# Performance work log

Hardware: AMD Instinct MI355X
Metric: run time of the kernel (lower is better)

## Reference

```python
import jax, jax.numpy as jnp
import numpy as np
from jax import lax

B, N, NUM_CLASSES = 16, 48384, 1
CONF_THRESH = 0.25
IOU_THRESH = 0.45
MAX_PER_IMG = 100
K = 512           # NMS candidate pool (top-K by score)
IMG_SIZE = 1536.0
CLS_OFFSET = 4096.0  # class-aware NMS offset trick


def setup_inputs() -> dict:
    key = jax.random.key(0)
    k1, k2, k3 = jax.random.split(key, 3)
    # cx, cy in [0, IMG), w, h in [0, 0.2*IMG)
    coords = jax.random.uniform(k1, (B, N, 4)) * jnp.array(
        [IMG_SIZE, IMG_SIZE, 0.2 * IMG_SIZE, 0.2 * IMG_SIZE], dtype=jnp.float32)
    confs = jax.random.uniform(k2, (B, N, 1 + NUM_CLASSES))  # obj + class scores in [0,1)
    pred_boxes = jnp.concatenate([coords, confs], axis=-1)   # [B, N, 6]
    features = jax.random.normal(k3, (B, 256, 48, 48), dtype=jnp.float32)
    return {"pred_boxes": pred_boxes, "features": features}


def _iou_matrix(boxes):
    # boxes: [K, 4] xyxy -> [K, K] pairwise IoU
    area = jnp.clip(boxes[:, 2] - boxes[:, 0], 0.0) * jnp.clip(boxes[:, 3] - boxes[:, 1], 0.0)
    lt = jnp.maximum(boxes[:, None, :2], boxes[None, :, :2])
    rb = jnp.minimum(boxes[:, None, 2:], boxes[None, :, 2:])
    wh = jnp.clip(rb - lt, 0.0)
    inter = wh[..., 0] * wh[..., 1]
    return inter / (area[:, None] + area[None, :] - inter + 1e-9)


def _find_thresh(scores, t0):
    # Retry loop of the wrapper: lower conf_thresh until >=1 box passes the conf mask.
    s = lax.stop_gradient(scores)
    def cond(t):
        return jnp.sum(s >= t) == 0
    def body(t):
        return jnp.maximum(t - 0.1, t / 10.0)
    return lax.while_loop(cond, body, t0)


def _postprocess_one(pred, thresh):
    # pred: [N, 5+num_classes]
    cx, cy, w, h = pred[:, 0], pred[:, 1], pred[:, 2], pred[:, 3]
    boxes = jnp.stack([cx - w / 2, cy - h / 2, cx + w / 2, cy + h / 2], axis=-1)  # xyxy
    obj = pred[:, 4]
    cls = pred[:, 5:]
    class_conf = jnp.max(cls, axis=-1)
    class_pred = jnp.argmax(cls, axis=-1)
    score = obj * class_conf
    valid = score >= thresh
    cand_score, idx = lax.top_k(jnp.where(valid, score, 0.0), K)
    cboxes = boxes[idx]
    ccls = class_pred[idx]
    cobj = obj[idx]
    cconf = class_conf[idx]
    cvalid = valid[idx]
    # class-aware NMS: offset boxes per class so cross-class pairs never overlap
    off = ccls.astype(boxes.dtype) * CLS_OFFSET
    iou = _iou_matrix(cboxes + off[:, None])  # [K, K]
    ar = jnp.arange(K)
    def body(i, keep):
        sup = keep[i] & (iou[i] > IOU_THRESH) & (ar > i)
        return keep & ~sup
    keep = lax.fori_loop(0, K, body, cvalid)  # greedy NMS (candidates sorted desc)
    final = jnp.where(keep, cand_score, 0.0)
    out_score, oidx = lax.top_k(final, MAX_PER_IMG)
    det = jnp.concatenate(
        [cboxes[oidx], cobj[oidx][:, None], cconf[oidx][:, None],
         ccls[oidx][:, None].astype(boxes.dtype)], axis=-1)  # [max_det, 7]
    kmask = keep[oidx]
    det = jnp.where(kmask[:, None], det, 0.0)
    return det, kmask


def reference(pred_boxes, features):
    obj = pred_boxes[..., 4]
    cconf = jnp.max(pred_boxes[..., 5:], axis=-1)
    scores = obj * cconf  # [B, N]
    t0 = jnp.full((pred_boxes.shape[0],), CONF_THRESH, pred_boxes.dtype)
    thresh = jax.vmap(_find_thresh)(scores, t0)
    det, mask = jax.vmap(_postprocess_one)(pred_boxes, thresh)
    return det, mask, features
```

## Files before the change

kernel.cpp:

```cpp
#include <hip/hip_runtime.h>
#include <stdint.h>

typedef unsigned int u32;
typedef unsigned long long u64;

#define BATCH 16
#define NBOX  48384
#define KC    512
#define MAXDET 100
#define CONF_T 0.25f
#define HCUT   0.75f
#define IOU_T  0.45f
#define DET_FLOATS (BATCH*MAXDET*7)
#define MASK_OFF   DET_FLOATS
#define FEAT_OFF   (DET_FLOATS + BATCH*MAXDET)
#define FEAT_N     (BATCH*256*48*48)
#define FEAT4_N    (FEAT_N/4)

#define CAPH  4096
#define HBUF  160
#define NBINS 64
#define NBLK1 64
#define BOXPB 756

#define F64   (FEAT4_N/64)
#define CSL1  (13*F64)
#define CSL2  (50*F64)
#define CSL3  (56*F64)
#define K1CPB  256
#define K2ACPB 480
#define K2BCPB 384
#define K2CCPB 240

__device__ __forceinline__ u64 xorred_u64(u64 v, int m){
    u32 lo = __shfl_xor((u32)(v & 0xFFFFFFFFull), m, 64);
    u32 hi = __shfl_xor((u32)(v >> 32), m, 64);
    return ((u64)hi << 32) | lo;
}
__device__ __forceinline__ u64 shflxor_u64(u64 v, int j){
    u32 lo = __shfl_xor((u32)(v & 0xFFFFFFFFull), j, 64);
    u32 hi = __shfl_xor((u32)(v >> 32), j, 64);
    return ((u64)hi << 32) | lo;
}
__device__ __forceinline__ u64 shflidx_u64(u64 v, int src){
    u32 lo = (u32)__shfl((int)(u32)(v & 0xFFFFFFFFull), src, 64);
    u32 hi = (u32)__shfl((int)(u32)(v >> 32), src, 64);
    return ((u64)hi << 32) | lo;
}
__device__ __forceinline__ int score_bin(float sc){
    int bin = (int)((sc - 0.75f) * 256.0f);
    return bin > 63 ? 63 : bin;
}

__global__ __launch_bounds__(512) void k1_score(const float* __restrict__ pred,
        u64* __restrict__ hkey, u32* __restrict__ blkcnt, u32* __restrict__ ghist,
        float* __restrict__ blkmax, const float4* __restrict__ feat4,
        float* __restrict__ out, int copyB)
{
    __shared__ u64 s_hb[HBUF];
    __shared__ u32 s_hist[NBINS];
    __shared__ u32 s_hc;
    __shared__ float s_wm[8];

    const int tid = threadIdx.x;

    if ((int)blockIdx.x < copyB){
        const int nthr = copyB * 512;
        float4* dst = reinterpret_cast<float4*>(out + FEAT_OFF);
        for (int i = (int)blockIdx.x*512 + tid; i < CSL1; i += nthr)
            dst[i] = feat4[i];
        return;
    }

    const int sid = (int)blockIdx.x - copyB;
    const int b = sid >> 6, blk = sid & 63;
    if (tid == 0) s_hc = 0u;
    if (tid < NBINS) s_hist[tid] = 0u;
    __syncthreads();

    const float* pb = pred + ((size_t)b*NBOX + (size_t)blk*BOXPB)*6;
    float m = 0.f;
    for (int i = tid; i < BOXPB; i += 512){
        const float2 oc = *(const float2*)(pb + (size_t)i*6 + 4);
        const float sc = oc.x * oc.y;
        m = fmaxf(m, sc);
        if (sc >= HCUT){
            const u32 slot = atomicAdd(&s_hc, 1u);
            const u32 idx = (u32)(blk*BOXPB + i);
            if (slot < (u32)HBUF)
                s_hb[slot] = ((u64)__float_as_uint(sc) << 32) | (u64)(0xFFFFFFFFu - idx);
            atomicAdd(&s_hist[score_bin(sc)], 1u);
        }
    }
    #pragma unroll
    for (int off = 32; off >= 1; off >>= 1) m = fmaxf(m, __shfl_xor(m, off, 64));
    if ((tid & 63) == 0) s_wm[tid >> 6] = m;
    __syncthreads();
    if (tid == 0){
        float mm = s_wm[0];
        #pragma unroll
        for (int w = 1; w < 8; w++) mm = fmaxf(mm, s_wm[w]);
        blkmax[sid] = mm;
        blkcnt[sid] = s_hc;
    }
    if (tid < NBINS) ghist[(size_t)sid*NBINS + tid] = s_hist[tid];
    const u32 hn = (s_hc < (u32)HBUF ? s_hc : (u32)HBUF);
    for (u32 i = tid; i < hn; i += 512)
        hkey[(size_t)sid*HBUF + i] = s_hb[i];
}

__global__ void copy_kernel(const float4* __restrict__ src, float4* __restrict__ dst){
    int stride = gridDim.x * blockDim.x;
    for (int i = blockIdx.x*blockDim.x + threadIdx.x; i < FEAT4_N; i += stride)
        dst[i] = src[i];
}

__global__ __launch_bounds__(512) void k2a_sel(
        const float* __restrict__ pred, const u64* __restrict__ hkey,
        const u32* __restrict__ blkcnt, u32* ghist ,
        const float* __restrict__ blkmax,
        const float4* __restrict__ feat4, float* __restrict__ out, int copyB)
{
    __shared__ u64 s_list[CAPH];
    __shared__ u64 s_key[KC];
    __shared__ u32 s_scr[1024];
    __shared__ u64 s_tie[256];
    __shared__ u32 s_eqidx[256];
    __shared__ u32 s_pfx[64], s_cnt[64];
    __shared__ float s_thresh;
    __shared__ u32 s_Mh, s_maxc, s_pivbin, s_need, s_fastok;
    __shared__ u32 s_prefix, s_k, s_cntgt, s_cnteq;
    __shared__ int s_vM;

    const int tid = threadIdx.x;

    if ((int)blockIdx.x >= BATCH){
        const int nthr = copyB * 512;
        float4* dst = reinterpret_cast<float4*>(out + FEAT_OFF);
        for (int i = CSL1 + ((int)blockIdx.x - BATCH)*512 + tid; i < CSL2; i += nthr)
            dst[i] = feat4[i];
        return;
    }

    const int b = blockIdx.x;
    const float* predb = pred + (size_t)b*NBOX*6;

    {
        if (tid < 64){
            float vv = blkmax[b*NBLK1 + tid];
            #pragma unroll
            for (int off = 32; off >= 1; off >>= 1) vv = fmaxf(vv, __shfl_xor(vv, off, 64));
            if (tid == 0){
                float t = CONF_T; int g = 0;
                while (vv < t && g < 256){ t = fmaxf(t - 0.1f, t * 0.1f); g++; }
                s_thresh = t;
                s_cntgt = 0u; s_cnteq = 0u; s_fastok = 0u;
            }
        } else if (tid < 128){
            const int l = tid - 64;
            u32 c = blkcnt[b*NBLK1 + l];
            s_cnt[l] = c;
            u32 p = c;
            #pragma unroll
            for (int off = 1; off < 64; off <<= 1){
                u32 o = __shfl_up(p, off, 64);
                if (l >= off) p += o;
            }
            s_pfx[l] = p - c;
            u32 mc = c;
            #pragma unroll
            for (int off = 32; off >= 1; off >>= 1) mc = (u32)max(mc, __shfl_xor(mc, off, 64));
            if (l == 63) s_Mh = p;
            if (l == 0)  s_maxc = mc;
        }
    }
    __syncthreads();
    const u32 Mh = s_Mh;
    const bool fastm = (Mh >= (u32)KC) && (Mh <= (u32)CAPH) && (s_maxc <= (u32)HBUF);

    if (fastm){
        const int wv = tid >> 6, ln = tid & 63;
        #pragma unroll
        for (int q = 0; q < 8; q++){
            const int s = wv + q*8;
            const u32 n = s_cnt[s], base = s_pfx[s];
            const u64* src = hkey + (size_t)(b*NBLK1 + s)*HBUF;
            for (u32 i = ln; i < n; i += 64) s_list[base + i] = src[i];
        }
        const int j = tid & 63, g = tid >> 6;
        const u32* gh = ghist + (size_t)b*NBLK1*NBINS;
        u32 acc = 0;
        #pragma unroll
        for (int r = 0; r < 8; r++) acc += gh[(g + r*8)*64 + j];
        s_scr[g*64 + j] = acc;
    }
    __syncthreads();
    if (fastm && tid < 64){
        u32 h = 0;
        #pragma unroll
        for (int g = 0; g < 8; g++) h += s_scr[g*64 + tid];
        u32 c = h;
        #pragma unroll
        for (int off = 1; off < 64; off <<= 1){
            u32 o = __shfl_down(c, off, 64);
            c += (tid + off < 64) ? o : 0u;
        }
        const u32 above = c - h;
        if (above < (u32)KC && above + h >= (u32)KC){
            s_pivbin = (u32)tid;
            s_need = (u32)KC - above;
            s_fastok = (h <= 256u) ? 1u : 0u;
        }
    }
    __syncthreads();
    const bool fsel = fastm && (s_fastok != 0u);

    if (fsel){
        const u32 pb = s_pivbin;
        const u32 lane = (u32)(tid & 63);
        const u64 below = (1ull << lane) - 1ull;
        for (u32 i0 = 0; i0 < Mh; i0 += 512){
            const u32 i = i0 + (u32)tid;
            const bool inr = (i < Mh);
            const u64 key = inr ? s_list[i] : 0ull;
            u32 j2 = 0u;
            if (inr){
                const float sc = __uint_as_float((u32)(key >> 32));
                j2 = (u32)score_bin(sc);
            }
            const bool isgt = inr && (j2 > pb);
            const bool iseq = inr && (j2 == pb);
            const u64 mg = __ballot(isgt);
            const u64 me = __ballot(iseq);
            u32 bg = 0u, be = 0u;
            if (lane == 0u){
                bg = atomicAdd(&s_cntgt, (u32)__popcll(mg));
                be = atomicAdd(&s_cnteq, (u32)__popcll(me));
            }
            bg = (u32)__shfl((int)bg, 0, 64);
            be = (u32)__shfl((int)be, 0, 64);
            if (isgt){
                const u32 sl = bg + (u32)__popcll(mg & below);
                if (sl < (u32)KC) s_key[sl] = key;
            } else if (iseq){
                const u32 e = be + (u32)__popcll(me & below);
                if (e < 256u) s_tie[e] = key;
            }
        }
        __syncthreads();
        {
            const u32 g0v = (s_cntgt < (u32)KC) ? s_cntgt : (u32)KC;
            u32 ecv = (s_cnteq < 256u) ? s_cnteq : 256u;
            u32 needv = (s_need < ecv) ? s_need : ecv;
            if (tid < (int)ecv){
                const u64 me2 = s_tie[tid];
                u32 r = 0;
                for (u32 u2 = 0; u2 < ecv; ++u2) r += (s_tie[u2] > me2) ? 1u : 0u;
                if (r < needv && g0v + r < (u32)KC) s_key[g0v + r] = me2;
            }
            for (int i = (int)(g0v + needv) + tid; i < KC; i += 512) s_key[i] = 0ull;
        }
        __syncthreads();
    } else {
        const float thresh = s_thresh;
        const u32 base8 = __float_as_uint(thresh) >> 24;
        u32 (*s_hist4)[256] = reinterpret_cast<u32(*)[256]>(s_scr);
        {
            u64 c0=0, c1=0, c2=0, c3=0;
            for (int i = tid; i < NBOX; i += 512){
                const float* pp = predb + (size_t)i*6;
                float sc = pp[4] * pp[5];
                if (sc >= thresh){
                    u32 d = (__float_as_uint(sc) >> 24) - base8; if (d > 15u) d = 15u;
                    u64 inc = 1ull << (16*(d & 3u)); u32 q = d >> 2;
                    c0 += (q==0u)?inc:0ull; c1 += (q==1u)?inc:0ull;
                    c2 += (q==2u)?inc:0ull; c3 += (q==3u)?inc:0ull;
                }
            }
            #pragma unroll
            for (int off = 32; off >= 1; off >>= 1){
                c0 += xorred_u64(c0,off); c1 += xorred_u64(c1,off);
                c2 += xorred_u64(c2,off); c3 += xorred_u64(c3,off);
            }
            u64* warr = s_key;
            if ((tid & 63) == 0){
                int w = tid >> 6;
                warr[w*4+0]=c0; warr[w*4+1]=c1; warr[w*4+2]=c2; warr[w*4+3]=c3;
            }
            __syncthreads();
            if (tid < 16){
                u32 tot = 0;
                #pragma unroll
                for (int w = 0; w < 8; w++){
                    u64 vv = warr[w*4 + (tid >> 2)];
                    tot += (u32)((vv >> (16*(tid & 3))) & 0xFFFFull);
                }
                s_hist4[0][tid] = tot;
            }
            __syncthreads();
            if (tid == 0){
                u32 h[16]; u32 tot = 0;
                #pragma unroll
                for (int d = 0; d < 16; d++){ h[d] = s_hist4[0][d]; tot += h[d]; }
                s_vM = (int)tot;
                s_k = KC; s_prefix = 0u;
                if (tot > (u32)KC){
                    u32 k = KC, c = 0; int d = 15;
                    for (; d >= 0; --d){ if (c + h[d] >= k) break; c += h[d]; }
                    if (d < 0) d = 0;
                    s_prefix = (base8 + (u32)d) << 24; s_k = k - c;
                }
            }
            __syncthreads();
        }
        const int vM = s_vM;
        if (vM > KC){
            for (int shift = 16; shift >= 0; shift -= 8){
                for (int z = tid; z < 1024; z += 512) ((u32*)s_hist4)[z] = 0u;
                __syncthreads();
                const u32 prefix = s_prefix;
                const u32 pmask = 0xFFFFFFFFu << (shift + 8);
                const int cpy = tid >> 8;
                for (int i = tid; i < NBOX; i += 512){
                    const float* pp = predb + (size_t)i*6;
                    float sc = pp[4] * pp[5];
                    if (sc >= thresh){
                        u32 bb = __float_as_uint(sc);
                        if ((bb & pmask) == (prefix & pmask))
                            atomicAdd(&s_hist4[cpy][(bb >> shift) & 0xFFu], 1u);
                    }
                }
                __syncthreads();
                if (tid < 256)
                    s_hist4[0][tid] = s_hist4[0][tid] + s_hist4[1][tid]
                                    + s_hist4[2][tid] + s_hist4[3][tid];
                __syncthreads();
                if (tid < 64){
                    const int l = tid;
                    u32 h0 = s_hist4[0][4*l+0], h1 = s_hist4[0][4*l+1];
                    u32 h2 = s_hist4[0][4*l+2], h3 = s_hist4[0][4*l+3];
                    u32 mysum = h0+h1+h2+h3;
                    u32 c = mysum;
                    #pragma unroll
                    for (int off = 1; off < 64; off <<= 1){
                        u32 o = __shfl_down(c, off, 64);
                        c += (l + off < 64) ? o : 0u;
                    }
                    u32 a3 = c - mysum;
                    u32 a2 = a3 + h3, a1 = a2 + h2, a0 = a1 + h1;
                    u32 k = s_k;
                    int sel = -1; u32 cab = 0;
                    if (a0 < k && a0 + h0 >= k){ sel = 0; cab = a0; }
                    if (a1 < k && a1 + h1 >= k){ sel = 1; cab = a1; }
                    if (a2 < k && a2 + h2 >= k){ sel = 2; cab = a2; }
                    if (a3 < k && a3 + h3 >= k){ sel = 3; cab = a3; }
                    if (sel >= 0){
                        s_prefix = prefix | ((u32)(4*l + sel) << shift);
                        s_k = k - cab;
                    }
                }
                __syncthreads();
            }
        }
        const u32 pivot = (vM > KC) ? s_prefix : 0u;
        const bool pivot0 = (vM <= KC);
        const int kneed = pivot0 ? 0 : (int)s_k;
        for (int i = tid; i < NBOX; i += 512){
            const float* pp = predb + (size_t)i*6;
            float sc = pp[4] * pp[5];
            if (sc < thresh) continue;
            u32 bb = __float_as_uint(sc);
            if (bb > pivot){
                u32 sl = atomicAdd(&s_cntgt, 1u);
                if (sl < (u32)KC) s_key[sl] = ((u64)bb << 32) | (u64)(0xFFFFFFFFu - (u32)i);
            } else if (!pivot0 && bb == pivot){
                u32 e = atomicAdd(&s_cnteq, 1u);
                if (e < 256u) s_eqidx[e] = (u32)i;
            }
        }
        __syncthreads();
        if (tid == 0){
            int g = (int)s_cntgt; if (g > KC) g = KC;
            int ec = (int)s_cnteq; if (ec > 256) ec = 256;
            int need = kneed < ec ? kneed : ec;
            for (int t = 0; t < need; t++){
                int mi = t;
                for (int u = t+1; u < ec; u++) if (s_eqidx[u] < s_eqidx[mi]) mi = u;
                u32 tmp = s_eqidx[mi]; s_eqidx[mi] = s_eqidx[t]; s_eqidx[t] = tmp;
                if (g < KC) s_key[g++] = ((u64)pivot << 32) | (u64)(0xFFFFFFFFu - tmp);
            }
            while (g < KC) s_key[g++] = 0ull;
        }
        __syncthreads();
    }

    u64 v = s_key[tid];
    {
        #define CAS_W(kk, j) \
            { \
                u64 p = shflxor_u64(v, (j)); \
                bool keepMax = (((tid & (kk)) == 0) == ((tid & (j)) == 0)); \
                u64 mx = (v > p) ? v : p, mn = (v > p) ? p : v; \
                v = keepMax ? mx : mn; \
            }
        #define CAS_L(kk, j) \
            __syncthreads(); \
            s_key[tid] = v; \
            __syncthreads(); \
            { \
                u64 p = s_key[tid ^ (j)]; \
                bool keepMax = (((tid & (kk)) == 0) == ((tid & (j)) == 0)); \
                u64 mx = (v > p) ? v : p, mn = (v > p) ? p : v; \
                v = keepMax ? mx : mn; \
            }
        CAS_W(2,1)
        CAS_W(4,2)  CAS_W(4,1)
        CAS_W(8,4)  CAS_W(8,2)  CAS_W(8,1)
        CAS_W(16,8) CAS_W(16,4) CAS_W(16,2) CAS_W(16,1)
        CAS_W(32,16) CAS_W(32,8) CAS_W(32,4) CAS_W(32,2) CAS_W(32,1)
        CAS_W(64,32) CAS_W(64,16) CAS_W(64,8) CAS_W(64,4) CAS_W(64,2) CAS_W(64,1)
        CAS_L(128,64)
        CAS_W(128,32) CAS_W(128,16) CAS_W(128,8) CAS_W(128,4) CAS_W(128,2) CAS_W(128,1)
        CAS_L(256,128) CAS_L(256,64)
        CAS_W(256,32) CAS_W(256,16) CAS_W(256,8) CAS_W(256,4) CAS_W(256,2) CAS_W(256,1)
        CAS_L(512,256) CAS_L(512,128) CAS_L(512,64)
        CAS_W(512,32) CAS_W(512,16) CAS_W(512,8) CAS_W(512,4) CAS_W(512,2) CAS_W(512,1)
        #undef CAS_W
        #undef CAS_L
    }

    {
        u32 bb = (u32)(v >> 32);
        u32 idx = 0xFFFFFFFFu - (u32)(v & 0xFFFFFFFFull);
        int srcrow = (bb != 0u) ? (int)idx : 0;
        const float* p = predb + (size_t)srcrow*6;
        const float2 p01 = *(const float2*)(p);
        const float2 p23 = *(const float2*)(p + 2);
        const float2 p45 = *(const float2*)(p + 4);
        float cx = p01.x, cy = p01.y, w = p23.x, h = p23.y, ob = p45.x, cf = p45.y;
        float x1 = cx - w * 0.5f, y1 = cy - h * 0.5f;
        float x2 = cx + w * 0.5f, y2 = cy + h * 0.5f;
        float4* cw = reinterpret_cast<float4*>(ghist) + ((size_t)b*KC + tid)*2;
        cw[0] = make_float4(x1, y1, x2, y2);
        cw[1] = make_float4(fmaxf(x2 - x1, 0.f) * fmaxf(y2 - y1, 0.f),
                            ob, cf, __uint_as_float(bb));
    }
}

__global__ __launch_bounds__(256) void k2b_iou(const float4* __restrict__ cand,
        u64* __restrict__ masks, u64* __restrict__ vmasks,
        const float4* __restrict__ feat4, float* __restrict__ out, int copyB)
{
    __shared__ float4 s_box[KC];
    __shared__ float s_area[KC];
    const int tid = threadIdx.x;

    if ((int)blockIdx.x >= BATCH*9){
        const int nthr = copyB * 256;
        float4* dst = reinterpret_cast<float4*>(out + FEAT_OFF);
        for (int i = CSL2 + ((int)blockIdx.x - BATCH*9)*256 + tid; i < CSL3; i += nthr)
            dst[i] = feat4[i];
        return;
    }

    const int b = (int)blockIdx.x / 9, q = (int)blockIdx.x % 9;
    const float4* cb = cand + (size_t)b*KC*2;

    for (int i = tid; i < KC; i += 256){
        s_box[i] = cb[2*i];
        s_area[i] = cb[2*i+1].x;
    }
    __syncthreads();

    const int wv = tid >> 6, lane = tid & 63;
    const int p = q*4 + wv;
    int d = 0; while ((d+1)*(d+2)/2 <= p) d++;
    const int c = p - d*(d+1)/2;
    const int j = d*64 + lane;
    const float4 bj = s_box[j];
    const float aj = s_area[j];
    const bool isdiag = (c == d);
    u64 acc = 0ull;
    for (int t = 0; t < 64; t++){
        const float4 bi = s_box[c*64 + t];
        const float ai = s_area[c*64 + t];
        float lx = fmaxf(bi.x, bj.x), ly = fmaxf(bi.y, bj.y);
        float rx = fminf(bi.z, bj.z), ry = fminf(bi.w, bj.w);
        float iw = fmaxf(rx - lx, 0.f), ih = fmaxf(ry - ly, 0.f);
        float inter = iw * ih;
        float denom = ai + aj - inter + 1e-9f;
        const bool iouc = (inter > IOU_T * denom);
        bool setb = isdiag ? (iouc && t > lane) : iouc;
        acc |= setb ? (1ull << t) : 0ull;
    }
    if (isdiag) vmasks[(size_t)b*KC + c*64 + lane] = acc;
    else        masks[(size_t)b*4096 + (size_t)c*512 + j] = acc;
}

__global__ __launch_bounds__(512) void k2c_nms(const float4* __restrict__ cand,
        const u64* __restrict__ masks, const u64* __restrict__ vmasks,
        float* __restrict__ out,
        const float4* __restrict__ feat4, int copyB)
{
    __shared__ u64 s_masks[8];
    __shared__ u32 s_wpcnt[8], s_wpfx[8];
    __shared__ int s_outidx[MAXDET];
    __shared__ int s_outcnt;

    const int tid = threadIdx.x;

    if ((int)blockIdx.x >= BATCH){
        const int nthr = copyB * 512;
        float4* dst = reinterpret_cast<float4*>(out + FEAT_OFF);
        for (int i = CSL3 + ((int)blockIdx.x - BATCH)*512 + tid; i < FEAT4_N; i += nthr)
            dst[i] = feat4[i];
        return;
    }

    const int b = blockIdx.x;
    const int wave = tid >> 6, lane = tid & 63;
    const float4* cb = cand + (size_t)b*KC*2;
    const u64* mb = masks + (size_t)b*4096;

    const float4 meta = cb[2*tid + 1];
    const bool alive0 = (__float_as_uint(meta.w) != 0u);
    const u64 vm = vmasks[(size_t)b*KC + tid];
    u64 pre[7];
    #pragma unroll
    for (int e = 0; e < 7; e++) pre[e] = (e < wave) ? mb[(size_t)e*512 + tid] : 0ull;

    for (int c = 0; c < 8; c++){
        if (wave == c){
            bool alive = alive0;
            #pragma unroll
            for (int e = 0; e < 7; e++)
                if (e < c) alive = alive && ((pre[e] & s_masks[e]) == 0ull);
            u64 A = __ballot(alive);
            #pragma unroll
            for (int t = 0; t < 64; t++){
                const u64 m = shflidx_u64(vm, t);
                if ((A >> t) & 1ull) A &= ~m;
            }
            if (lane == 0) s_masks[c] = A;
        }
        __syncthreads();
    }

    if (tid < 8) s_wpcnt[tid] = (u32)__popcll(s_masks[tid]);
    __syncthreads();
    if (tid == 0){
        u32 run = 0;
        #pragma unroll
        for (int w = 0; w < 8; w++){ s_wpfx[w] = run; run += s_wpcnt[w]; }
        s_outcnt = (int)(run < MAXDET ? run : MAXDET);
    }
    __syncthreads();
    {
        const u64 wd = s_masks[wave];
        if ((wd >> lane) & 1ull){
            u32 rank = s_wpfx[wave] + (u32)__popcll(wd & ((1ull << lane) - 1ull));
            if (rank < MAXDET) s_outidx[rank] = tid;
        }
    }
    __syncthreads();
    if (tid < MAXDET){
        const int obase = (b * MAXDET + tid) * 7;
        if (tid < s_outcnt){
            int c = s_outidx[tid];
            float4 bx = cb[2*c];
            float4 mt = cb[2*c + 1];
            out[obase+0] = bx.x; out[obase+1] = bx.y;
            out[obase+2] = bx.z; out[obase+3] = bx.w;
            out[obase+4] = mt.y; out[obase+5] = mt.z;
            out[obase+6] = 0.f;
            out[MASK_OFF + b*MAXDET + tid] = 1.f;
        } else {
            #pragma unroll
            for (int q = 0; q < 7; q++) out[obase+q] = 0.f;
            out[MASK_OFF + b*MAXDET + tid] = 0.f;
        }
    }
}

extern "C" void kernel_launch(void* const* d_in, const int* in_sizes, int n_in,
                              void* d_out, int out_size, void* d_ws, size_t ws_size,
                              hipStream_t stream) {
    (void)in_sizes; (void)n_in; (void)out_size;
    const float* pred = (const float*)d_in[0];
    const float* feat = (const float*)d_in[1];
    float* out = (float*)d_out;

    const size_t hkeyBytes = (size_t)BATCH * NBLK1 * HBUF * 8;
    const size_t cntBytes  = (size_t)BATCH * NBLK1 * 4;
    const size_t histBytes = (size_t)BATCH * NBLK1 * NBINS * 4;
    const size_t maxBytes  = (size_t)BATCH * NBLK1 * 4;
    const size_t needBytes = hkeyBytes + cntBytes + histBytes + maxBytes;

    char* base; bool fused;
    if (ws_size >= needBytes){ base = (char*)d_ws; fused = true; }
    else { base = (char*)(out + FEAT_OFF); fused = false; }

    u64* hkeyp  = (u64*)base;
    u32* blkcnt = (u32*)(base + hkeyBytes);
    u32* ghist  = (u32*)(base + hkeyBytes + cntBytes);
    float* blkmax = (float*)(base + hkeyBytes + cntBytes + histBytes);
    float4* cand = (float4*)ghist;
    u64* masks   = hkeyp;
    u64* vmasks  = hkeyp + (size_t)BATCH*4096;

    if (fused){
        k1_score<<<dim3(K1CPB + BATCH*NBLK1), dim3(512), 0, stream>>>(
            pred, hkeyp, blkcnt, ghist, blkmax, (const float4*)feat, out, K1CPB);
        k2a_sel<<<dim3(BATCH + K2ACPB), dim3(512), 0, stream>>>(
            pred, hkeyp, blkcnt, ghist, blkmax, (const float4*)feat, out, K2ACPB);
        k2b_iou<<<dim3(BATCH*9 + K2BCPB), dim3(256), 0, stream>>>(
            cand, masks, vmasks, (const float4*)feat, out, K2BCPB);
        k2c_nms<<<dim3(BATCH + K2CCPB), dim3(512), 0, stream>>>(
            cand, masks, vmasks, out, (const float4*)feat, K2CCPB);
    } else {
        k1_score<<<dim3(BATCH*NBLK1), dim3(512), 0, stream>>>(
            pred, hkeyp, blkcnt, ghist, blkmax, (const float4*)feat, out, 0);
        k2a_sel<<<dim3(BATCH), dim3(512), 0, stream>>>(
            pred, hkeyp, blkcnt, ghist, blkmax, (const float4*)feat, out, 0);
        k2b_iou<<<dim3(BATCH*9), dim3(256), 0, stream>>>(
            cand, masks, vmasks, (const float4*)feat, out, 0);
        k2c_nms<<<dim3(BATCH), dim3(512), 0, stream>>>(
            cand, masks, vmasks, out, (const float4*)feat, 0);
        copy_kernel<<<dim3(1024), dim3(256), 0, stream>>>(
            (const float4*)feat, (float4*)(out + FEAT_OFF));
    }
}
```

Measured before the change: 134.3 us.

## Fuse selection, IoU mask and NMS kernels into one with per-batch flag sync

Merges the top-K selection, pairwise IoU bitmask, and greedy NMS kernels into one kernel. Each image gets 8 blocks that all redo the selection: seven compute off-diagonal IoU mask tiles and signal an atomic flag, while the lead block computes the diagonal masks and spins on that flag before running NMS. The feature copy is also repartitioned across two launches instead of four. This removes two kernel launches and the global candidate round trip. The cost is redundant selection work across 8 blocks per image and a spin-wait that assumes all blocks of an image are resident together.

Result: slower. 150.5 us (+12.1%).

```diff
diff --git a/kernel.cpp b/kernel.cpp
--- a/kernel.cpp
+++ b/kernel.cpp
@@ -22,15 +22,12 @@
 #define NBINS 64
 #define NBLK1 64
 #define BOXPB 756
+#define NCOMP 8
 
 #define F64   (FEAT4_N/64)
-#define CSL1  (13*F64)
-#define CSL2  (50*F64)
-#define CSL3  (56*F64)
-#define K1CPB  256
-#define K2ACPB 480
-#define K2BCPB 384
-#define K2CCPB 240
+#define CSLK1 (24*F64)
+#define K1CPB 256
+#define K2CPB 384
 
 __device__ __forceinline__ u64 xorred_u64(u64 v, int m){
     u32 lo = __shfl_xor((u32)(v & 0xFFFFFFFFull), m, 64);
@@ -54,8 +51,8 @@
 
 __global__ __launch_bounds__(512) void k1_score(const float* __restrict__ pred,
         u64* __restrict__ hkey, u32* __restrict__ blkcnt, u32* __restrict__ ghist,
-        float* __restrict__ blkmax, const float4* __restrict__ feat4,
-        float* __restrict__ out, int copyB)
+        float* __restrict__ blkmax, u32* __restrict__ flags,
+        const float4* __restrict__ feat4, float* __restrict__ out, int copyB)
 {
     __shared__ u64 s_hb[HBUF];
     __shared__ u32 s_hist[NBINS];
@@ -67,13 +64,14 @@
     if ((int)blockIdx.x < copyB){
         const int nthr = copyB * 512;
         float4* dst = reinterpret_cast<float4*>(out + FEAT_OFF);
-        for (int i = (int)blockIdx.x*512 + tid; i < CSL1; i += nthr)
+        for (int i = (int)blockIdx.x*512 + tid; i < CSLK1; i += nthr)
             dst[i] = feat4[i];
         return;
     }
 
     const int sid = (int)blockIdx.x - copyB;
     const int b = sid >> 6, blk = sid & 63;
+    if (sid == 0 && tid < BATCH) flags[tid] = 0u;
     if (tid == 0) s_hc = 0u;
     if (tid < NBINS) s_hist[tid] = 0u;
     __syncthreads();
@@ -115,10 +113,11 @@
         dst[i] = src[i];
 }
 
-__global__ __launch_bounds__(512) void k2a_sel(
+__global__ __launch_bounds__(512) void k2_fused(
         const float* __restrict__ pred, const u64* __restrict__ hkey,
-        const u32* __restrict__ blkcnt, u32* ghist ,
+        const u32* __restrict__ blkcnt, const u32* __restrict__ ghist,
         const float* __restrict__ blkmax,
+        u64* __restrict__ masks, u32* __restrict__ flags,
         const float4* __restrict__ feat4, float* __restrict__ out, int copyB)
 {
     __shared__ u64 s_list[CAPH];
@@ -127,23 +126,32 @@
     __shared__ u64 s_tie[256];
     __shared__ u32 s_eqidx[256];
     __shared__ u32 s_pfx[64], s_cnt[64];
+    __shared__ float4 s_box[KC];
+    __shared__ float s_area[KC];
+    __shared__ float s_obj[KC];
+    __shared__ float s_conf[KC];
+    __shared__ u64 s_masks[8];
+    __shared__ u32 s_wpcnt[8], s_wpfx[8];
+    __shared__ int s_outidx[MAXDET];
     __shared__ float s_thresh;
     __shared__ u32 s_Mh, s_maxc, s_pivbin, s_need, s_fastok;
     __shared__ u32 s_prefix, s_k, s_cntgt, s_cnteq;
-    __shared__ int s_vM;
+    __shared__ int s_vM, s_outcnt;
 
     const int tid = threadIdx.x;
 
-    if ((int)blockIdx.x >= BATCH){
+    if ((int)blockIdx.x >= BATCH*NCOMP){
         const int nthr = copyB * 512;
         float4* dst = reinterpret_cast<float4*>(out + FEAT_OFF);
-        for (int i = CSL1 + ((int)blockIdx.x - BATCH)*512 + tid; i < CSL2; i += nthr)
+        for (int i = CSLK1 + ((int)blockIdx.x - BATCH*NCOMP)*512 + tid; i < FEAT4_N; i += nthr)
             dst[i] = feat4[i];
         return;
     }
 
-    const int b = blockIdx.x;
+    const int b = (int)blockIdx.x >> 3;
+    const int role = (int)blockIdx.x & 7;
     const float* predb = pred + (size_t)b*NBOX*6;
+    u64* masksb = masks + (size_t)b*4096;
 
     {
         if (tid < 64){
@@ -440,94 +448,69 @@
         float cx = p01.x, cy = p01.y, w = p23.x, h = p23.y, ob = p45.x, cf = p45.y;
         float x1 = cx - w * 0.5f, y1 = cy - h * 0.5f;
         float x2 = cx + w * 0.5f, y2 = cy + h * 0.5f;
-        float4* cw = reinterpret_cast<float4*>(ghist) + ((size_t)b*KC + tid)*2;
-        cw[0] = make_float4(x1, y1, x2, y2);
-        cw[1] = make_float4(fmaxf(x2 - x1, 0.f) * fmaxf(y2 - y1, 0.f),
-                            ob, cf, __uint_as_float(bb));
-    }
-}
-
-__global__ __launch_bounds__(256) void k2b_iou(const float4* __restrict__ cand,
-        u64* __restrict__ masks, u64* __restrict__ vmasks,
-        const float4* __restrict__ feat4, float* __restrict__ out, int copyB)
-{
-    __shared__ float4 s_box[KC];
-    __shared__ float s_area[KC];
-    const int tid = threadIdx.x;
-
-    if ((int)blockIdx.x >= BATCH*9){
-        const int nthr = copyB * 256;
-        float4* dst = reinterpret_cast<float4*>(out + FEAT_OFF);
-        for (int i = CSL2 + ((int)blockIdx.x - BATCH*9)*256 + tid; i < CSL3; i += nthr)
-            dst[i] = feat4[i];
+        s_box[tid] = make_float4(x1, y1, x2, y2);
+        s_area[tid] = fmaxf(x2 - x1, 0.f) * fmaxf(y2 - y1, 0.f);
+        s_obj[tid] = ob; s_conf[tid] = cf;
+    }
+    __syncthreads();
+
+    const int wave = tid >> 6, lane = tid & 63;
+
+    if (role != 0){
+        if (wave < 4){
+            const int p = (role - 1)*4 + wave;
+            int d = 1; while ((d+1)*d/2 <= p) d++;
+            const int c = p - d*(d-1)/2;
+            const int j = d*64 + lane;
+            const float4 bj = s_box[j];
+            const float aj = s_area[j];
+            u64 acc = 0ull;
+            for (int t = 0; t < 64; t++){
+                const float4 bi = s_box[c*64 + t];
+                const float ai = s_area[c*64 + t];
+                float lx = fmaxf(bi.x, bj.x), ly = fmaxf(bi.y, bj.y);
+                float rx = fminf(bi.z, bj.z), ry = fminf(bi.w, bj.w);
+                float iw = fmaxf(rx - lx, 0.f), ih = fmaxf(ry - ly, 0.f);
+                float inter = iw * ih;
+                float denom = ai + aj - inter + 1e-9f;
+                bool sup = (inter > IOU_T * denom);
+                acc |= sup ? (1ull << t) : 0ull;
+            }
+            masksb[(size_t)c*512 + j] = acc;
+        }
+        __threadfence();
+        __syncthreads();
+        if (tid == 0) atomicAdd(&flags[b], 1u);
         return;
     }
 
-    const int b = (int)blockIdx.x / 9, q = (int)blockIdx.x % 9;
-    const float4* cb = cand + (size_t)b*KC*2;
-
-    for (int i = tid; i < KC; i += 256){
-        s_box[i] = cb[2*i];
-        s_area[i] = cb[2*i+1].x;
-    }
-    __syncthreads();
-
-    const int wv = tid >> 6, lane = tid & 63;
-    const int p = q*4 + wv;
-    int d = 0; while ((d+1)*(d+2)/2 <= p) d++;
-    const int c = p - d*(d+1)/2;
-    const int j = d*64 + lane;
-    const float4 bj = s_box[j];
-    const float aj = s_area[j];
-    const bool isdiag = (c == d);
-    u64 acc = 0ull;
-    for (int t = 0; t < 64; t++){
-        const float4 bi = s_box[c*64 + t];
-        const float ai = s_area[c*64 + t];
-        float lx = fmaxf(bi.x, bj.x), ly = fmaxf(bi.y, bj.y);
-        float rx = fminf(bi.z, bj.z), ry = fminf(bi.w, bj.w);
-        float iw = fmaxf(rx - lx, 0.f), ih = fmaxf(ry - ly, 0.f);
-        float inter = iw * ih;
-        float denom = ai + aj - inter + 1e-9f;
-        const bool iouc = (inter > IOU_T * denom);
-        bool setb = isdiag ? (iouc && t > lane) : iouc;
-        acc |= setb ? (1ull << t) : 0ull;
-    }
-    if (isdiag) vmasks[(size_t)b*KC + c*64 + lane] = acc;
-    else        masks[(size_t)b*4096 + (size_t)c*512 + j] = acc;
-}
-
-__global__ __launch_bounds__(512) void k2c_nms(const float4* __restrict__ cand,
-        const u64* __restrict__ masks, const u64* __restrict__ vmasks,
-        float* __restrict__ out,
-        const float4* __restrict__ feat4, int copyB)
-{
-    __shared__ u64 s_masks[8];
-    __shared__ u32 s_wpcnt[8], s_wpfx[8];
-    __shared__ int s_outidx[MAXDET];
-    __shared__ int s_outcnt;
-
-    const int tid = threadIdx.x;
-
-    if ((int)blockIdx.x >= BATCH){
-        const int nthr = copyB * 512;
-        float4* dst = reinterpret_cast<float4*>(out + FEAT_OFF);
-        for (int i = CSL3 + ((int)blockIdx.x - BATCH)*512 + tid; i < FEAT4_N; i += nthr)
-            dst[i] = feat4[i];
-        return;
-    }
-
-    const int b = blockIdx.x;
-    const int wave = tid >> 6, lane = tid & 63;
-    const float4* cb = cand + (size_t)b*KC*2;
-    const u64* mb = masks + (size_t)b*4096;
-
-    const float4 meta = cb[2*tid + 1];
-    const bool alive0 = (__float_as_uint(meta.w) != 0u);
-    const u64 vm = vmasks[(size_t)b*KC + tid];
+    u64 vm = 0ull;
+    {
+        const float4 bj = s_box[wave*64 + lane];
+        const float aj = s_area[wave*64 + lane];
+        for (int t = 0; t < 64; t++){
+            const float4 bi = s_box[wave*64 + t];
+            const float ai = s_area[wave*64 + t];
+            float lx = fmaxf(bi.x, bj.x), ly = fmaxf(bi.y, bj.y);
+            float rx = fminf(bi.z, bj.z), ry = fminf(bi.w, bj.w);
+            float iw = fmaxf(rx - lx, 0.f), ih = fmaxf(ry - ly, 0.f);
+            float inter = iw * ih;
+            float denom = aj + ai - inter + 1e-9f;
+            bool sup = (inter > IOU_T * denom) && (t > lane);
+            vm |= sup ? (1ull << t) : 0ull;
+        }
+    }
+    const bool alive0 = (((u32)(v >> 32)) != 0u);
+
+    if (tid == 0){
+        while (atomicAdd(&flags[b], 0u) < 7u){ }
+    }
+    __syncthreads();
+    __threadfence();
+
     u64 pre[7];
     #pragma unroll
-    for (int e = 0; e < 7; e++) pre[e] = (e < wave) ? mb[(size_t)e*512 + tid] : 0ull;
+    for (int e = 0; e < 7; e++) pre[e] = (e < wave) ? masksb[(size_t)e*512 + tid] : 0ull;
 
     for (int c = 0; c < 8; c++){
         if (wave == c){
@@ -567,11 +550,10 @@
         const int obase = (b * MAXDET + tid) * 7;
         if (tid < s_outcnt){
             int c = s_outidx[tid];
-            float4 bx = cb[2*c];
-            float4 mt = cb[2*c + 1];
+            float4 bx = s_box[c];
             out[obase+0] = bx.x; out[obase+1] = bx.y;
             out[obase+2] = bx.z; out[obase+3] = bx.w;
-            out[obase+4] = mt.y; out[obase+5] = mt.z;
+            out[obase+4] = s_obj[c]; out[obase+5] = s_conf[c];
             out[obase+6] = 0.f;
             out[MASK_OFF + b*MAXDET + tid] = 1.f;
         } else {
@@ -594,7 +576,10 @@
     const size_t cntBytes  = (size_t)BATCH * NBLK1 * 4;
     const size_t histBytes = (size_t)BATCH * NBLK1 * NBINS * 4;
     const size_t maxBytes  = (size_t)BATCH * NBLK1 * 4;
-    const size_t needBytes = hkeyBytes + cntBytes + histBytes + maxBytes;
+    const size_t flagBytes = 64;
+    const size_t maskBytes = (size_t)BATCH * 4096 * 8;
+    const size_t needBytes = hkeyBytes + cntBytes + histBytes + maxBytes
+                           + flagBytes + maskBytes;
 
     char* base; bool fused;
     if (ws_size >= needBytes){ base = (char*)d_ws; fused = true; }
@@ -604,28 +589,21 @@
     u32* blkcnt = (u32*)(base + hkeyBytes);
     u32* ghist  = (u32*)(base + hkeyBytes + cntBytes);
     float* blkmax = (float*)(base + hkeyBytes + cntBytes + histBytes);
-    float4* cand = (float4*)ghist;
-    u64* masks   = hkeyp;
-    u64* vmasks  = hkeyp + (size_t)BATCH*4096;
+    u32* flags  = (u32*)(base + hkeyBytes + cntBytes + histBytes + maxBytes);
+    u64* masks  = (u64*)(base + hkeyBytes + cntBytes + histBytes + maxBytes + flagBytes);
 
     if (fused){
         k1_score<<<dim3(K1CPB + BATCH*NBLK1), dim3(512), 0, stream>>>(
-            pred, hkeyp, blkcnt, ghist, blkmax, (const float4*)feat, out, K1CPB);
-        k2a_sel<<<dim3(BATCH + K2ACPB), dim3(512), 0, stream>>>(
-            pred, hkeyp, blkcnt, ghist, blkmax, (const float4*)feat, out, K2ACPB);
-        k2b_iou<<<dim3(BATCH*9 + K2BCPB), dim3(256), 0, stream>>>(
-            cand, masks, vmasks, (const float4*)feat, out, K2BCPB);
-        k2c_nms<<<dim3(BATCH + K2CCPB), dim3(512), 0, stream>>>(
-            cand, masks, vmasks, out, (const float4*)feat, K2CCPB);
+            pred, hkeyp, blkcnt, ghist, blkmax, flags, (const float4*)feat, out, K1CPB);
+        k2_fused<<<dim3(BATCH*NCOMP + K2CPB), dim3(512), 0, stream>>>(
+            pred, hkeyp, blkcnt, ghist, blkmax, masks, flags,
+            (const float4*)feat, out, K2CPB);
     } else {
         k1_score<<<dim3(BATCH*NBLK1), dim3(512), 0, stream>>>(
-            pred, hkeyp, blkcnt, ghist, blkmax, (const float4*)feat, out, 0);
-        k2a_sel<<<dim3(BATCH), dim3(512), 0, stream>>>(
-            pred, hkeyp, blkcnt, ghist, blkmax, (const float4*)feat, out, 0);
-        k2b_iou<<<dim3(BATCH*9), dim3(256), 0, stream>>>(
-            cand, masks, vmasks, (const float4*)feat, out, 0);
-        k2c_nms<<<dim3(BATCH), dim3(512), 0, stream>>>(
-            cand, masks, vmasks, out, (const float4*)feat, 0);
+            pred, hkeyp, blkcnt, ghist, blkmax, flags, (const float4*)feat, out, 0);
+        k2_fused<<<dim3(BATCH*NCOMP), dim3(512), 0, stream>>>(
+            pred, hkeyp, blkcnt, ghist, blkmax, masks, flags,
+            (const float4*)feat, out, 0);
         copy_kernel<<<dim3(1024), dim3(256), 0, stream>>>(
             (const float4*)feat, (float4*)(out + FEAT_OFF));
     }
```

## Fuse IoU-mask and NMS kernels, stream candidates directly, replace bitonic sort with rank sort

Applied to the files above, without the earlier changes.

Merges the IoU bitmask kernel and the greedy NMS kernel into one launch. Each image's block now computes the 36 triangular 64x64 tiles into shared memory, so the masks no longer round-trip through global memory. The selection kernel scans per-block candidate keys straight from global memory instead of staging them into a shared list first. The 512-element bitonic sort is replaced by an O(K) rank-count scatter per thread. The feature-copy slices are redistributed across the remaining three launches. This removes a kernel launch and global traffic, but IoU work now runs on only 16 blocks instead of 144, and the rank sort does 512 shared reads per thread.

New measurement: 167.7 us. +24.9%, slower.

```diff
diff --git a/kernel.cpp b/kernel.cpp
--- a/kernel.cpp
+++ b/kernel.cpp
@@ -24,22 +24,15 @@
 #define BOXPB 756
 
 #define F64   (FEAT4_N/64)
-#define CSL1  (13*F64)
-#define CSL2  (50*F64)
-#define CSL3  (56*F64)
+#define CSL1  (32*F64)
+#define CSL2  (48*F64)
 #define K1CPB  256
-#define K2ACPB 480
-#define K2BCPB 384
-#define K2CCPB 240
+#define K2ACPB 368
+#define K2BCPB 368
 
 __device__ __forceinline__ u64 xorred_u64(u64 v, int m){
     u32 lo = __shfl_xor((u32)(v & 0xFFFFFFFFull), m, 64);
     u32 hi = __shfl_xor((u32)(v >> 32), m, 64);
-    return ((u64)hi << 32) | lo;
-}
-__device__ __forceinline__ u64 shflxor_u64(u64 v, int j){
-    u32 lo = __shfl_xor((u32)(v & 0xFFFFFFFFull), j, 64);
-    u32 hi = __shfl_xor((u32)(v >> 32), j, 64);
     return ((u64)hi << 32) | lo;
 }
 __device__ __forceinline__ u64 shflidx_u64(u64 v, int src){
@@ -121,12 +114,11 @@
         const float* __restrict__ blkmax,
         const float4* __restrict__ feat4, float* __restrict__ out, int copyB)
 {
-    __shared__ u64 s_list[CAPH];
     __shared__ u64 s_key[KC];
     __shared__ u32 s_scr[1024];
     __shared__ u64 s_tie[256];
     __shared__ u32 s_eqidx[256];
-    __shared__ u32 s_pfx[64], s_cnt[64];
+    __shared__ u32 s_cnt[64];
     __shared__ float s_thresh;
     __shared__ u32 s_Mh, s_maxc, s_pivbin, s_need, s_fastok;
     __shared__ u32 s_prefix, s_k, s_cntgt, s_cnteq;
@@ -160,18 +152,13 @@
             const int l = tid - 64;
             u32 c = blkcnt[b*NBLK1 + l];
             s_cnt[l] = c;
-            u32 p = c;
+            u32 sum = c;
             #pragma unroll
-            for (int off = 1; off < 64; off <<= 1){
-                u32 o = __shfl_up(p, off, 64);
-                if (l >= off) p += o;
-            }
-            s_pfx[l] = p - c;
+            for (int off = 32; off >= 1; off >>= 1) sum += __shfl_xor(sum, off, 64);
             u32 mc = c;
             #pragma unroll
             for (int off = 32; off >= 1; off >>= 1) mc = (u32)max(mc, __shfl_xor(mc, off, 64));
-            if (l == 63) s_Mh = p;
-            if (l == 0)  s_maxc = mc;
+            if (l == 0){ s_Mh = sum; s_maxc = mc; }
         }
     }
     __syncthreads();
@@ -179,14 +166,6 @@
     const bool fastm = (Mh >= (u32)KC) && (Mh <= (u32)CAPH) && (s_maxc <= (u32)HBUF);
 
     if (fastm){
-        const int wv = tid >> 6, ln = tid & 63;
-        #pragma unroll
-        for (int q = 0; q < 8; q++){
-            const int s = wv + q*8;
-            const u32 n = s_cnt[s], base = s_pfx[s];
-            const u64* src = hkey + (size_t)(b*NBLK1 + s)*HBUF;
-            for (u32 i = ln; i < n; i += 64) s_list[base + i] = src[i];
-        }
         const int j = tid & 63, g = tid >> 6;
         const u32* gh = ghist + (size_t)b*NBLK1*NBINS;
         u32 acc = 0;
@@ -217,34 +196,41 @@
 
     if (fsel){
         const u32 pb = s_pivbin;
+        const int wv = tid >> 6;
         const u32 lane = (u32)(tid & 63);
         const u64 below = (1ull << lane) - 1ull;
-        for (u32 i0 = 0; i0 < Mh; i0 += 512){
-            const u32 i = i0 + (u32)tid;
-            const bool inr = (i < Mh);
-            const u64 key = inr ? s_list[i] : 0ull;
-            u32 j2 = 0u;
-            if (inr){
-                const float sc = __uint_as_float((u32)(key >> 32));
-                j2 = (u32)score_bin(sc);
-            }
-            const bool isgt = inr && (j2 > pb);
-            const bool iseq = inr && (j2 == pb);
-            const u64 mg = __ballot(isgt);
-            const u64 me = __ballot(iseq);
-            u32 bg = 0u, be = 0u;
-            if (lane == 0u){
-                bg = atomicAdd(&s_cntgt, (u32)__popcll(mg));
-                be = atomicAdd(&s_cnteq, (u32)__popcll(me));
-            }
-            bg = (u32)__shfl((int)bg, 0, 64);
-            be = (u32)__shfl((int)be, 0, 64);
-            if (isgt){
-                const u32 sl = bg + (u32)__popcll(mg & below);
-                if (sl < (u32)KC) s_key[sl] = key;
-            } else if (iseq){
-                const u32 e = be + (u32)__popcll(me & below);
-                if (e < 256u) s_tie[e] = key;
+        #pragma unroll
+        for (int q = 0; q < 8; q++){
+            const int s = wv*8 + q;
+            const u32 n = s_cnt[s];
+            const u64* src = hkey + (size_t)(b*NBLK1 + s)*HBUF;
+            for (u32 i0 = 0; i0 < n; i0 += 64){
+                const u32 i = i0 + lane;
+                const bool inr = (i < n);
+                const u64 key = inr ? src[i] : 0ull;
+                u32 j2 = 0u;
+                if (inr){
+                    const float sc = __uint_as_float((u32)(key >> 32));
+                    j2 = (u32)score_bin(sc);
+                }
+                const bool isgt = inr && (j2 > pb);
+                const bool iseq = inr && (j2 == pb);
+                const u64 mg = __ballot(isgt);
+                const u64 me = __ballot(iseq);
+                u32 bg = 0u, be = 0u;
+                if (lane == 0u){
+                    bg = atomicAdd(&s_cntgt, (u32)__popcll(mg));
+                    be = atomicAdd(&s_cnteq, (u32)__popcll(me));
+                }
+                bg = (u32)__shfl((int)bg, 0, 64);
+                be = (u32)__shfl((int)be, 0, 64);
+                if (isgt){
+                    const u32 sl = bg + (u32)__popcll(mg & below);
+                    if (sl < (u32)KC) s_key[sl] = key;
+                } else if (iseq){
+                    const u32 e = be + (u32)__popcll(me & below);
+                    if (e < 256u) s_tie[e] = key;
+                }
             }
         }
         __syncthreads();
@@ -394,39 +380,19 @@
         __syncthreads();
     }
 
-    u64 v = s_key[tid];
+    u64 v;
     {
-        #define CAS_W(kk, j) \
-            { \
-                u64 p = shflxor_u64(v, (j)); \
-                bool keepMax = (((tid & (kk)) == 0) == ((tid & (j)) == 0)); \
-                u64 mx = (v > p) ? v : p, mn = (v > p) ? p : v; \
-                v = keepMax ? mx : mn; \
-            }
-        #define CAS_L(kk, j) \
-            __syncthreads(); \
-            s_key[tid] = v; \
-            __syncthreads(); \
-            { \
-                u64 p = s_key[tid ^ (j)]; \
-                bool keepMax = (((tid & (kk)) == 0) == ((tid & (j)) == 0)); \
-                u64 mx = (v > p) ? v : p, mn = (v > p) ? p : v; \
-                v = keepMax ? mx : mn; \
-            }
-        CAS_W(2,1)
-        CAS_W(4,2)  CAS_W(4,1)
-        CAS_W(8,4)  CAS_W(8,2)  CAS_W(8,1)
-        CAS_W(16,8) CAS_W(16,4) CAS_W(16,2) CAS_W(16,1)
-        CAS_W(32,16) CAS_W(32,8) CAS_W(32,4) CAS_W(32,2) CAS_W(32,1)
-        CAS_W(64,32) CAS_W(64,16) CAS_W(64,8) CAS_W(64,4) CAS_W(64,2) CAS_W(64,1)
-        CAS_L(128,64)
-        CAS_W(128,32) CAS_W(128,16) CAS_W(128,8) CAS_W(128,4) CAS_W(128,2) CAS_W(128,1)
-        CAS_L(256,128) CAS_L(256,64)
-        CAS_W(256,32) CAS_W(256,16) CAS_W(256,8) CAS_W(256,4) CAS_W(256,2) CAS_W(256,1)
-        CAS_L(512,256) CAS_L(512,128) CAS_L(512,64)
-        CAS_W(512,32) CAS_W(512,16) CAS_W(512,8) CAS_W(512,4) CAS_W(512,2) CAS_W(512,1)
-        #undef CAS_W
-        #undef CAS_L
+        const u64 me2 = s_key[tid];
+        u32 r = 0;
+        #pragma unroll 8
+        for (int u = 0; u < KC; u++){
+            const u64 o = s_key[u];
+            r += (o > me2 || (o == me2 && u < tid)) ? 1u : 0u;
+        }
+        u64* s_out = reinterpret_cast<u64*>(s_scr);
+        s_out[r] = me2;
+        __syncthreads();
+        v = s_out[tid];
     }
 
     {
@@ -447,61 +413,15 @@
     }
 }
 
-__global__ __launch_bounds__(256) void k2b_iou(const float4* __restrict__ cand,
-        u64* __restrict__ masks, u64* __restrict__ vmasks,
-        const float4* __restrict__ feat4, float* __restrict__ out, int copyB)
+__global__ __launch_bounds__(512) void k2bc_nms(const float4* __restrict__ cand,
+        float* __restrict__ out, const float4* __restrict__ feat4, int copyB)
 {
     __shared__ float4 s_box[KC];
     __shared__ float s_area[KC];
-    const int tid = threadIdx.x;
-
-    if ((int)blockIdx.x >= BATCH*9){
-        const int nthr = copyB * 256;
-        float4* dst = reinterpret_cast<float4*>(out + FEAT_OFF);
-        for (int i = CSL2 + ((int)blockIdx.x - BATCH*9)*256 + tid; i < CSL3; i += nthr)
-            dst[i] = feat4[i];
-        return;
-    }
-
-    const int b = (int)blockIdx.x / 9, q = (int)blockIdx.x % 9;
-    const float4* cb = cand + (size_t)b*KC*2;
-
-    for (int i = tid; i < KC; i += 256){
-        s_box[i] = cb[2*i];
-        s_area[i] = cb[2*i+1].x;
-    }
-    __syncthreads();
-
-    const int wv = tid >> 6, lane = tid & 63;
-    const int p = q*4 + wv;
-    int d = 0; while ((d+1)*(d+2)/2 <= p) d++;
-    const int c = p - d*(d+1)/2;
-    const int j = d*64 + lane;
-    const float4 bj = s_box[j];
-    const float aj = s_area[j];
-    const bool isdiag = (c == d);
-    u64 acc = 0ull;
-    for (int t = 0; t < 64; t++){
-        const float4 bi = s_box[c*64 + t];
-        const float ai = s_area[c*64 + t];
-        float lx = fmaxf(bi.x, bj.x), ly = fmaxf(bi.y, bj.y);
-        float rx = fminf(bi.z, bj.z), ry = fminf(bi.w, bj.w);
-        float iw = fmaxf(rx - lx, 0.f), ih = fmaxf(ry - ly, 0.f);
-        float inter = iw * ih;
-        float denom = ai + aj - inter + 1e-9f;
-        const bool iouc = (inter > IOU_T * denom);
-        bool setb = isdiag ? (iouc && t > lane) : iouc;
-        acc |= setb ? (1ull << t) : 0ull;
-    }
-    if (isdiag) vmasks[(size_t)b*KC + c*64 + lane] = acc;
-    else        masks[(size_t)b*4096 + (size_t)c*512 + j] = acc;
-}
-
-__global__ __launch_bounds__(512) void k2c_nms(const float4* __restrict__ cand,
-        const u64* __restrict__ masks, const u64* __restrict__ vmasks,
-        float* __restrict__ out,
-        const float4* __restrict__ feat4, int copyB)
-{
+    __shared__ float s_obj[KC];
+    __shared__ float s_conf[KC];
+    __shared__ u64 s_off[28*64];
+    __shared__ u64 s_vm[KC];
     __shared__ u64 s_masks[8];
     __shared__ u32 s_wpcnt[8], s_wpfx[8];
     __shared__ int s_outidx[MAXDET];
@@ -512,29 +432,55 @@
     if ((int)blockIdx.x >= BATCH){
         const int nthr = copyB * 512;
         float4* dst = reinterpret_cast<float4*>(out + FEAT_OFF);
-        for (int i = CSL3 + ((int)blockIdx.x - BATCH)*512 + tid; i < FEAT4_N; i += nthr)
+        for (int i = CSL2 + ((int)blockIdx.x - BATCH)*512 + tid; i < FEAT4_N; i += nthr)
             dst[i] = feat4[i];
         return;
     }
 
     const int b = blockIdx.x;
+    const float4* cb = cand + (size_t)b*KC*2;
+
+    const float4 bx0 = cb[2*tid];
+    const float4 mt0 = cb[2*tid + 1];
+    s_box[tid] = bx0;
+    s_area[tid] = mt0.x;
+    s_obj[tid] = mt0.y;
+    s_conf[tid] = mt0.z;
+    const bool alive0 = (__float_as_uint(mt0.w) != 0u);
+    __syncthreads();
+
     const int wave = tid >> 6, lane = tid & 63;
-    const float4* cb = cand + (size_t)b*KC*2;
-    const u64* mb = masks + (size_t)b*4096;
-
-    const float4 meta = cb[2*tid + 1];
-    const bool alive0 = (__float_as_uint(meta.w) != 0u);
-    const u64 vm = vmasks[(size_t)b*KC + tid];
-    u64 pre[7];
-    #pragma unroll
-    for (int e = 0; e < 7; e++) pre[e] = (e < wave) ? mb[(size_t)e*512 + tid] : 0ull;
-
+
+    for (int p = wave; p < 36; p += 8){
+        int d = 0; while ((d+1)*(d+2)/2 <= p) d++;
+        const int c = p - d*(d+1)/2;
+        const float4 bj = s_box[d*64 + lane];
+        const float aj = s_area[d*64 + lane];
+        const bool isdiag = (c == d);
+        u64 acc = 0ull;
+        for (int t = 0; t < 64; t++){
+            const float4 bi = s_box[c*64 + t];
+            const float ai = s_area[c*64 + t];
+            float lx = fmaxf(bi.x, bj.x), ly = fmaxf(bi.y, bj.y);
+            float rx = fminf(bi.z, bj.z), ry = fminf(bi.w, bj.w);
+            float iw = fmaxf(rx - lx, 0.f), ih = fmaxf(ry - ly, 0.f);
+            float inter = iw * ih;
+            float denom = ai + aj - inter + 1e-9f;
+            const bool iouc = (inter > IOU_T * denom);
+            bool setb = isdiag ? (iouc && t > lane) : iouc;
+            acc |= setb ? (1ull << t) : 0ull;
+        }
+        if (isdiag) s_vm[c*64 + lane] = acc;
+        else        s_off[(d*(d-1)/2 + c)*64 + lane] = acc;
+    }
+    __syncthreads();
+
+    const u64 vm = s_vm[wave*64 + lane];
     for (int c = 0; c < 8; c++){
         if (wave == c){
             bool alive = alive0;
-            #pragma unroll
-            for (int e = 0; e < 7; e++)
-                if (e < c) alive = alive && ((pre[e] & s_masks[e]) == 0ull);
+            for (int e = 0; e < c; e++)
+                alive = alive && ((s_off[(c*(c-1)/2 + e)*64 + lane] & s_masks[e]) == 0ull);
             u64 A = __ballot(alive);
             #pragma unroll
             for (int t = 0; t < 64; t++){
@@ -567,11 +513,10 @@
         const int obase = (b * MAXDET + tid) * 7;
         if (tid < s_outcnt){
             int c = s_outidx[tid];
-            float4 bx = cb[2*c];
-            float4 mt = cb[2*c + 1];
+            float4 bx = s_box[c];
             out[obase+0] = bx.x; out[obase+1] = bx.y;
             out[obase+2] = bx.z; out[obase+3] = bx.w;
-            out[obase+4] = mt.y; out[obase+5] = mt.z;
+            out[obase+4] = s_obj[c]; out[obase+5] = s_conf[c];
             out[obase+6] = 0.f;
             out[MASK_OFF + b*MAXDET + tid] = 1.f;
         } else {
@@ -605,27 +550,21 @@
     u32* ghist  = (u32*)(base + hkeyBytes + cntBytes);
     float* blkmax = (float*)(base + hkeyBytes + cntBytes + histBytes);
     float4* cand = (float4*)ghist;
-    u64* masks   = hkeyp;
-    u64* vmasks  = hkeyp + (size_t)BATCH*4096;
 
     if (fused){
         k1_score<<<dim3(K1CPB + BATCH*NBLK1), dim3(512), 0, stream>>>(
             pred, hkeyp, blkcnt, ghist, blkmax, (const float4*)feat, out, K1CPB);
         k2a_sel<<<dim3(BATCH + K2ACPB), dim3(512), 0, stream>>>(
             pred, hkeyp, blkcnt, ghist, blkmax, (const float4*)feat, out, K2ACPB);
-        k2b_iou<<<dim3(BATCH*9 + K2BCPB), dim3(256), 0, stream>>>(
-            cand, masks, vmasks, (const float4*)feat, out, K2BCPB);
-        k2c_nms<<<dim3(BATCH + K2CCPB), dim3(512), 0, stream>>>(
-            cand, masks, vmasks, out, (const float4*)feat, K2CCPB);
+        k2bc_nms<<<dim3(BATCH + K2BCPB), dim3(512), 0, stream>>>(
+            cand, out, (const float4*)feat, K2BCPB);
     } else {
         k1_score<<<dim3(BATCH*NBLK1), dim3(512), 0, stream>>>(
             pred, hkeyp, blkcnt, ghist, blkmax, (const float4*)feat, out, 0);
         k2a_sel<<<dim3(BATCH), dim3(512), 0, stream>>>(
             pred, hkeyp, blkcnt, ghist, blkmax, (const float4*)feat, out, 0);
-        k2b_iou<<<dim3(BATCH*9), dim3(256), 0, stream>>>(
-            cand, masks, vmasks, (const float4*)feat, out, 0);
-        k2c_nms<<<dim3(BATCH), dim3(512), 0, stream>>>(
-            cand, masks, vmasks, out, (const float4*)feat, 0);
+        k2bc_nms<<<dim3(BATCH), dim3(512), 0, stream>>>(
+            cand, out, (const float4*)feat, 0);
         copy_kernel<<<dim3(1024), dim3(256), 0, stream>>>(
             (const float4*)feat, (float4*)(out + FEAT_OFF));
     }
```
